# Kernel tuning notes

Hardware: AMD Instinct MI355X
Metric: run time of the kernel (lower is better)

Reference implementation:

```python
import jax, jax.numpy as jnp
import numpy as np

B, S, H = 2, 2048, 2048
NH = 16
HD = H // NH  # 128


def setup_inputs() -> dict:
    key = jax.random.key(0)
    ks = jax.random.split(key, 6)
    sc = 0.02
    return {
        "x": jax.random.normal(ks[0], (B, S, H), dtype=jnp.float32),
        "attention_mask": jnp.zeros((B, S), dtype=jnp.float32),
        "Wq": jax.random.normal(ks[1], (H, H), dtype=jnp.float32) * sc,
        "bq": jnp.zeros((H,), dtype=jnp.float32),
        "Wk": jax.random.normal(ks[2], (H, H), dtype=jnp.float32) * sc,
        "bk": jnp.zeros((H,), dtype=jnp.float32),
        "Wv": jax.random.normal(ks[3], (H, H), dtype=jnp.float32) * sc,
        "bv": jnp.zeros((H,), dtype=jnp.float32),
        "Wo": jax.random.normal(ks[4], (H, H), dtype=jnp.float32) * sc,
        "bo": jnp.zeros((H,), dtype=jnp.float32),
    }


def reference(x, attention_mask, Wq, bq, Wk, bk, Wv, bv, Wo, bo):
    b, s, h = x.shape
    q = (x @ Wq + bq).reshape(b, s, NH, HD)
    k = (x @ Wk + bk).reshape(b, s, NH, HD)
    v = (x @ Wv + bv).reshape(b, s, NH, HD)
    scale = 1.0 / jnp.sqrt(jnp.asarray(HD, dtype=x.dtype))
    scores = jnp.einsum('bqhd,bkhd->bhqk', q, k) * scale
    scores = scores + attention_mask[:, None, None, :]
    weights = jax.nn.softmax(scores, axis=-1)
    attn = jnp.einsum('bhqk,bkhd->bqhd', weights, v).reshape(b, s, h)
    return attn @ Wo + bo
```

## Files before the change

kernel.cpp:

```cpp
#include <hip/hip_runtime.h>
#include <hip/hip_bf16.h>
#include <stdint.h>

#define BB   2
#define SS   2048
#define HHH  2048
#define NHH  16
#define HDD  128
#define MTOT 4096

typedef __bf16 bf16x8 __attribute__((ext_vector_type(8)));
typedef float  f32x4  __attribute__((ext_vector_type(4)));
typedef float  f32x16 __attribute__((ext_vector_type(16)));

#define MFMA16(a, b, c) __builtin_amdgcn_mfma_f32_16x16x32_bf16((a), (b), (c), 0, 0, 0)
#define MFMA32(a, b, c) __builtin_amdgcn_mfma_f32_32x32x16_bf16((a), (b), (c), 0, 0, 0)

__device__ __forceinline__ unsigned short f2bf(float f) {
    union { float f; unsigned u; } v; v.f = f;
    unsigned r = v.u + 0x7FFFu + ((v.u >> 16) & 1u);
    return (unsigned short)(r >> 16);
}

__device__ __forceinline__ unsigned packbf(float a, float b) {
    union { __bf16 h[2]; unsigned u; } p;
    p.h[0] = (__bf16)a; p.h[1] = (__bf16)b;
    return p.u;
}

__device__ __forceinline__ void pswap(unsigned &a, unsigned &b) {
    asm("v_permlane32_swap_b32 %0, %1" : "+v"(a), "+v"(b));
}

__device__ __forceinline__ float2 xswap(float x) {
    unsigned a = __builtin_bit_cast(unsigned, x);
    unsigned b;
    asm("v_mov_b32 %0, %1" : "=v"(b) : "v"(a));
    asm("v_permlane32_swap_b32 %0, %1" : "+v"(a), "+v"(b));
    return make_float2(__builtin_bit_cast(float, a), __builtin_bit_cast(float, b));
}

__device__ __forceinline__ void gload16(const void* src, void* lds) {
    __builtin_amdgcn_global_load_lds(
        (__attribute__((address_space(1))) void*)src,
        (__attribute__((address_space(3))) void*)lds,
        16, 0, 0);
}

__global__ void cast_f32_bf16(const float* __restrict__ in,
                              unsigned short* __restrict__ out, int n) {
    int i = (blockIdx.x * blockDim.x + threadIdx.x) * 4;
    int stride = gridDim.x * blockDim.x * 4;
    for (; i < n; i += stride) {
        float4 v = *(const float4*)(in + i);
        ushort4 o;
        o.x = f2bf(v.x); o.y = f2bf(v.y); o.z = f2bf(v.z); o.w = f2bf(v.w);
        *(ushort4*)(out + i) = o;
    }
}

__global__ void scale_mask(const float* __restrict__ in, float* __restrict__ out) {
    int i = blockIdx.x * 256 + threadIdx.x;
    out[i] = in[i] * 1.4426950408889634f;
}

__global__ void transpose_cast4(const float* __restrict__ W0, const float* __restrict__ W1,
                                const float* __restrict__ W2, const float* __restrict__ W3,
                                unsigned short* __restrict__ out) {
    const float* in = blockIdx.z == 0 ? W0 : blockIdx.z == 1 ? W1 : blockIdx.z == 2 ? W2 : W3;
    unsigned short* o = out + (size_t)blockIdx.z * ((size_t)HHH * HHH);
    __shared__ float tile[32][33];
    int c0 = blockIdx.x * 32, r0 = blockIdx.y * 32;
    int tx = threadIdx.x, ty = threadIdx.y;
    #pragma unroll
    for (int i = 0; i < 32; i += 8)
        tile[ty + i][tx] = in[(size_t)(r0 + ty + i) * HHH + c0 + tx];
    __syncthreads();
    #pragma unroll
    for (int i = 0; i < 32; i += 8)
        o[(size_t)(c0 + ty + i) * HHH + r0 + tx] = f2bf(tile[tx][ty + i]);
}

template<int MODE>
__global__ __launch_bounds__(512, 2) void gemm8_bf16(
    const unsigned short* __restrict__ A,
    const unsigned short* __restrict__ Bt,
    const float* __restrict__ bias,
    void* __restrict__ Cout,
    int M, int N, int K)
{
    __shared__ __align__(16) unsigned char sm[147456];
    const int tid = threadIdx.x;
    const int wv = tid >> 6, ln = tid & 63;
    const int g = ln >> 4, r = ln & 15;
    const int wr = wv >> 2, wc = wv & 3;

    const int bid = blockIdx.x;
    const int lb = (bid & 7) * 32 + (bid >> 3);
    const int m0 = (lb & 31) * 128;
    const int n0 = (lb >> 5) * 256;

    unsigned srcA[2]; int ldsA[2];
    #pragma unroll
    for (int j = 0; j < 2; ++j) {
        int o = j * 8192 + tid * 16;
        int row = o >> 7;
        int lg = ((o >> 4) & 7) ^ (row & 7);
        srcA[j] = (unsigned)(m0 + row) * K + lg * 8;
        ldsA[j] = o;
    }
    unsigned srcB[4]; int ldsB[4];
    #pragma unroll
    for (int j = 0; j < 4; ++j) {
        int o = j * 8192 + tid * 16;
        int row = o >> 7;
        int lg = ((o >> 4) & 7) ^ (row & 7);
        srcB[j] = (unsigned)(n0 + row) * K + lg * 8;
        ldsB[j] = 16384 + o;
    }

    f32x4 acc[4][4];
    #pragma unroll
    for (int i = 0; i < 4; ++i)
        #pragma unroll
        for (int j = 0; j < 4; ++j)
            acc[i][j] = (f32x4){0.f, 0.f, 0.f, 0.f};

    const int NT = K >> 6;

    {
        unsigned char* b0 = sm;
        unsigned char* b1 = sm + 49152;
        #pragma unroll
        for (int j = 0; j < 2; ++j) gload16(A + srcA[j], b0 + ldsA[j]);
        #pragma unroll
        for (int j = 0; j < 4; ++j) gload16(Bt + srcB[j], b0 + ldsB[j]);
        #pragma unroll
        for (int j = 0; j < 2; ++j) gload16(A + srcA[j] + 64, b1 + ldsA[j]);
        #pragma unroll
        for (int j = 0; j < 4; ++j) gload16(Bt + srcB[j] + 64, b1 + ldsB[j]);
    }
    asm volatile("s_waitcnt vmcnt(6)" ::: "memory");
    __builtin_amdgcn_s_barrier();

    int csel = 0;
    int psel = 2;
    for (int t = 0; t < NT; ++t) {
        const unsigned char* Ab = sm + csel * 49152;
        const unsigned char* Bb = Ab + 16384;
        unsigned char* Pb = sm + psel * 49152;
        const bool pre = (t + 2 < NT);
        const int ko = (t + 2) * 64;

        bf16x8 af[2][2], bf[2][2];
        #define LDA(mi, ks) (*(const bf16x8*)(Ab + (wr * 64 + (mi) * 16 + r) * 128 + \
                             ((((ks) << 2) + g) ^ ((wr * 64 + (mi) * 16 + r) & 7)) * 16))
        #define LDB(ni, ks) (*(const bf16x8*)(Bb + (wc * 64 + (ni) * 16 + r) * 128 + \
                             ((((ks) << 2) + g) ^ ((wc * 64 + (ni) * 16 + r) & 7)) * 16))

        af[0][0] = LDA(0, 0); af[0][1] = LDA(0, 1);
        af[1][0] = LDA(1, 0); af[1][1] = LDA(1, 1);
        bf[0][0] = LDB(0, 0); bf[0][1] = LDB(0, 1);
        bf[1][0] = LDB(1, 0); bf[1][1] = LDB(1, 1);
        if (pre) { gload16(Bt + srcB[0] + ko, Pb + ldsB[0]);
                   gload16(Bt + srcB[1] + ko, Pb + ldsB[1]); }
        __builtin_amdgcn_s_barrier();
        asm volatile("s_waitcnt lgkmcnt(0)" ::: "memory");
        __builtin_amdgcn_s_setprio(1);
        #pragma unroll
        for (int mi = 0; mi < 2; ++mi)
            #pragma unroll
            for (int ni = 0; ni < 2; ++ni)
                #pragma unroll
                for (int ks = 0; ks < 2; ++ks)
                    acc[mi][ni] = MFMA16(af[mi][ks], bf[ni][ks], acc[mi][ni]);
        __builtin_amdgcn_s_setprio(0);
        __builtin_amdgcn_s_barrier();

        bf[0][0] = LDB(2, 0); bf[0][1] = LDB(2, 1);
        bf[1][0] = LDB(3, 0); bf[1][1] = LDB(3, 1);
        if (pre) { gload16(Bt + srcB[2] + ko, Pb + ldsB[2]);
                   gload16(Bt + srcB[3] + ko, Pb + ldsB[3]); }
        __builtin_amdgcn_s_barrier();
        asm volatile("s_waitcnt lgkmcnt(0)" ::: "memory");
        __builtin_amdgcn_s_setprio(1);
        #pragma unroll
        for (int mi = 0; mi < 2; ++mi)
            #pragma unroll
            for (int ni = 0; ni < 2; ++ni)
                #pragma unroll
                for (int ks = 0; ks < 2; ++ks)
                    acc[mi][ni + 2] = MFMA16(af[mi][ks], bf[ni][ks], acc[mi][ni + 2]);
        __builtin_amdgcn_s_setprio(0);
        __builtin_amdgcn_s_barrier();

        af[0][0] = LDA(2, 0); af[0][1] = LDA(2, 1);
        af[1][0] = LDA(3, 0); af[1][1] = LDA(3, 1);
        if (pre) { gload16(A + srcA[0] + ko, Pb + ldsA[0]);
                   gload16(A + srcA[1] + ko, Pb + ldsA[1]); }
        __builtin_amdgcn_s_barrier();
        asm volatile("s_waitcnt lgkmcnt(0)" ::: "memory");
        __builtin_amdgcn_s_setprio(1);
        #pragma unroll
        for (int mi = 0; mi < 2; ++mi)
            #pragma unroll
            for (int ni = 0; ni < 2; ++ni)
                #pragma unroll
                for (int ks = 0; ks < 2; ++ks)
                    acc[mi + 2][ni + 2] = MFMA16(af[mi][ks], bf[ni][ks], acc[mi + 2][ni + 2]);
        __builtin_amdgcn_s_setprio(0);
        __builtin_amdgcn_s_barrier();

        bf[0][0] = LDB(0, 0); bf[0][1] = LDB(0, 1);
        bf[1][0] = LDB(1, 0); bf[1][1] = LDB(1, 1);
        __builtin_amdgcn_s_barrier();
        asm volatile("s_waitcnt lgkmcnt(0)" ::: "memory");
        __builtin_amdgcn_s_setprio(1);
        #pragma unroll
        for (int mi = 0; mi < 2; ++mi)
            #pragma unroll
            for (int ni = 0; ni < 2; ++ni)
                #pragma unroll
                for (int ks = 0; ks < 2; ++ks)
                    acc[mi + 2][ni] = MFMA16(af[mi][ks], bf[ni][ks], acc[mi + 2][ni]);
        __builtin_amdgcn_s_setprio(0);
        __builtin_amdgcn_s_barrier();

        if (pre) asm volatile("s_waitcnt vmcnt(6)" ::: "memory");
        else     asm volatile("s_waitcnt vmcnt(0)" ::: "memory");
        __builtin_amdgcn_s_barrier();

        csel = (csel == 2) ? 0 : csel + 1;
        psel = (psel == 2) ? 0 : psel + 1;
        #undef LDA
        #undef LDB
    }

    #pragma unroll
    for (int mt = 0; mt < 4; ++mt) {
        #pragma unroll
        for (int nt = 0; nt < 4; ++nt) {
            int col = n0 + wc * 64 + nt * 16 + r;
            float bvv = bias[col];
            f32x4 a = acc[mt][nt];
            int mrow = m0 + wr * 64 + mt * 16 + g * 4;
            if (MODE == 0) {
                #pragma unroll
                for (int q = 0; q < 4; ++q)
                    ((unsigned short*)Cout)[(size_t)(mrow + q) * N + col] = f2bf(a[q] + bvv);
            } else if (MODE == 2) {
                #pragma unroll
                for (int q = 0; q < 4; ++q)
                    ((float*)Cout)[(size_t)(mrow + q) * N + col] = a[q] + bvv;
            } else {
                int b = mrow >> 11, s0x = mrow & 2047;
                ushort4 o;
                o.x = f2bf(a[0] + bvv); o.y = f2bf(a[1] + bvv);
                o.z = f2bf(a[2] + bvv); o.w = f2bf(a[3] + bvv);
                *(ushort4*)((unsigned short*)Cout + ((size_t)(b * 2048 + col)) * 2048 + s0x) = o;
            }
        }
    }
}

__global__ __launch_bounds__(256, 2) void attn_fwd(
    const unsigned short* __restrict__ Q,
    const unsigned short* __restrict__ K,
    const unsigned short* __restrict__ V,
    const float* __restrict__ maskl2,
    unsigned short* __restrict__ O)
{
    __shared__ __align__(16) unsigned char sm[49152];
    const int tid = threadIdx.x, wv = tid >> 6, ln = tid & 63;
    const int hi = ln >> 5, qr = ln & 31;

    const int bid = blockIdx.x;
    const int lb = (bid & 7) * 64 + (bid >> 3);
    const int qb = lb & 15;
    const int bh = lb >> 4;
    const int h = bh & 15, b = bh >> 4;

    const size_t rowQ0 = (size_t)(b * 2048 + qb * 128 + wv * 32);
    const float SCL2 = 0.08838834764831845f * 1.4426950408889634f;

    unsigned srcK[2], srcV[2];
    int ldsK[2], ldsV[2];
    #pragma unroll
    for (int i = 0; i < 2; ++i) {
        int ch = wv * 2 + i;
        int o = ch * 1024 + ln * 16;
        { int row = o >> 8; int gl = ((o >> 4) & 15) ^ (row & 7);
          srcK[i] = (unsigned)((b * 2048 + row) * 2048 + h * 128 + gl * 8);
          ldsK[i] = o; }
        { int d = o >> 6; int gl = ((o >> 4) & 3) ^ ((d >> 1) & 3);
          srcV[i] = (unsigned)((b * 2048 + h * 128 + d) * 2048 + gl * 8);
          ldsV[i] = 8192 + o; }
    }

    #define STAGE(t, base) { \
        _Pragma("unroll") \
        for (int i = 0; i < 2; ++i) { \
            gload16(K + srcK[i] + (unsigned)(t) * (32u * 2048u), sm + (base) + ldsK[i]); \
            gload16(V + srcV[i] + (unsigned)(t) * 32u, sm + (base) + ldsV[i]); \
        } }

    STAGE(0, 0); STAGE(1, 16384); STAGE(2, 32768);

    bf16x8 qf[8];
    #pragma unroll
    for (int ks = 0; ks < 8; ++ks)
        qf[ks] = *(const bf16x8*)(Q + (rowQ0 + qr) * 2048 + h * 128 + ks * 16 + hi * 8);

    f32x16 acc[4];
    #pragma unroll
    for (int i = 0; i < 4; ++i)
        #pragma unroll
        for (int j = 0; j < 16; ++j)
            acc[i][j] = 0.f;
    float mr = -3.0e38f, lr = 0.f;

    const float* mb = maskl2 + b * 2048;

    asm volatile("s_waitcnt vmcnt(8)" ::: "memory");
    __builtin_amdgcn_s_barrier();

    int bufo = 0;
    for (int t = 0; t < 64; ++t) {
        const unsigned char* Kt = sm + bufo;
        const unsigned char* Vt = Kt + 8192;

        f32x4 mk[4];
        #pragma unroll
        for (int rg = 0; rg < 4; ++rg)
            mk[rg] = *(const f32x4*)(mb + t * 32 + rg * 8 + hi * 4);

        f32x16 sf;
        #pragma unroll
        for (int j = 0; j < 16; ++j) sf[j] = 0.f;
        __builtin_amdgcn_s_setprio(1);
        #pragma unroll
        for (int ks = 0; ks < 8; ++ks) {
            int s0 = (2 * ks + hi) ^ (qr & 7);
            bf16x8 kf = *(const bf16x8*)(Kt + qr * 256 + s0 * 16);
            sf = MFMA32(kf, qf[ks], sf);
        }
        __builtin_amdgcn_s_setprio(0);

        float sv[16];
        #pragma unroll
        for (int reg = 0; reg < 16; ++reg)
            sv[reg] = sf[reg] * SCL2 + mk[reg >> 2][reg & 3];

        float mx[8];
        #pragma unroll
        for (int j = 0; j < 8; ++j)
            mx[j] = fmaxf(sv[2 * j], sv[2 * j + 1]);
        float m01 = fmaxf(fmaxf(fmaxf(mx[0], mx[1]), fmaxf(mx[2], mx[3])),
                          fmaxf(fmaxf(mx[4], mx[5]), fmaxf(mx[6], mx[7])));
        float2 mp = xswap(m01);
        float mt = fmaxf(mp.x, mp.y);

        float alpha = 1.f;
        int allskip = __all(mt <= mr + 8.f);
        if (!allskip) {
            float nm = fmaxf(mr, mt);
            alpha = __builtin_amdgcn_exp2f(mr - nm);
            mr = nm;
            #pragma unroll
            for (int dblk = 0; dblk < 4; ++dblk)
                #pragma unroll
                for (int reg = 0; reg < 16; ++reg)
                    acc[dblk][reg] *= alpha;
        }

        float s0 = 0.f, s1 = 0.f, s2 = 0.f, s3 = 0.f;
        #pragma unroll
        for (int reg = 0; reg < 16; reg += 4) {
            float p0 = __builtin_amdgcn_exp2f(sv[reg + 0] - mr);
            float p1 = __builtin_amdgcn_exp2f(sv[reg + 1] - mr);
            float p2 = __builtin_amdgcn_exp2f(sv[reg + 2] - mr);
            float p3 = __builtin_amdgcn_exp2f(sv[reg + 3] - mr);
            sv[reg + 0] = p0; sv[reg + 1] = p1;
            sv[reg + 2] = p2; sv[reg + 3] = p3;
            s0 += p0; s1 += p1; s2 += p2; s3 += p3;
        }
        float rsl = (s0 + s1) + (s2 + s3);
        float2 rp = xswap(rsl);
        float rs = rp.x + rp.y;
        lr = lr * alpha + rs;

        bf16x8 pfr[2];
        #pragma unroll
        for (int kb16 = 0; kb16 < 2; ++kb16) {
            unsigned W00 = packbf(sv[(2*kb16+0)*4 + 0], sv[(2*kb16+0)*4 + 1]);
            unsigned W01 = packbf(sv[(2*kb16+0)*4 + 2], sv[(2*kb16+0)*4 + 3]);
            unsigned W10 = packbf(sv[(2*kb16+1)*4 + 0], sv[(2*kb16+1)*4 + 1]);
            unsigned W11 = packbf(sv[(2*kb16+1)*4 + 2], sv[(2*kb16+1)*4 + 3]);
            pswap(W00, W10);
            pswap(W01, W11);
            union { unsigned w[4]; bf16x8 v; } u;
            u.w[0] = W00; u.w[1] = W01; u.w[2] = W10; u.w[3] = W11;
            pfr[kb16] = u.v;
        }

        __builtin_amdgcn_s_setprio(1);
        #pragma unroll
        for (int dblk = 0; dblk < 4; ++dblk) {
            int d = dblk * 32 + qr;
            f32x16 a = acc[dblk];
            #pragma unroll
            for (int kb16 = 0; kb16 < 2; ++kb16) {
                int s = (2 * kb16 + hi) ^ ((d >> 1) & 3);
                bf16x8 vf = *(const bf16x8*)(Vt + d * 64 + s * 16);
                a = MFMA32(vf, pfr[kb16], a);
            }
            acc[dblk] = a;
        }
        __builtin_amdgcn_s_setprio(0);

        asm volatile("s_waitcnt vmcnt(4)" ::: "memory");
        __builtin_amdgcn_s_barrier();

        if (t + 3 < 64) STAGE(t + 3, bufo);
        bufo = (bufo == 32768) ? 0 : bufo + 16384;
    }

    float linv = 1.f / lr;
    unsigned short* orow = O + (rowQ0 + qr) * 2048 + h * 128;
    #pragma unroll
    for (int dblk = 0; dblk < 4; ++dblk)
        #pragma unroll
        for (int rg = 0; rg < 4; ++rg) {
            float v0 = acc[dblk][rg * 4 + 0] * linv;
            float v1 = acc[dblk][rg * 4 + 1] * linv;
            float v2 = acc[dblk][rg * 4 + 2] * linv;
            float v3 = acc[dblk][rg * 4 + 3] * linv;
            uint2 o;
            o.x = packbf(v0, v1);
            o.y = packbf(v2, v3);
            *(uint2*)(orow + dblk * 32 + rg * 8 + hi * 4) = o;
        }
    #undef STAGE
}

extern "C" void kernel_launch(void* const* d_in, const int* in_sizes, int n_in,
                              void* d_out, int out_size, void* d_ws, size_t ws_size,
                              hipStream_t stream)
{
    (void)in_sizes; (void)n_in; (void)out_size; (void)ws_size;
    const float* x    = (const float*)d_in[0];
    const float* mask = (const float*)d_in[1];
    const float* Wq   = (const float*)d_in[2];
    const float* bq   = (const float*)d_in[3];
    const float* Wk   = (const float*)d_in[4];
    const float* bk   = (const float*)d_in[5];
    const float* Wv   = (const float*)d_in[6];
    const float* bv   = (const float*)d_in[7];
    const float* Wo   = (const float*)d_in[8];
    const float* bo   = (const float*)d_in[9];
    float* out = (float*)d_out;

    char* ws = (char*)d_ws;
    unsigned short* xb  = (unsigned short*)(ws);
    unsigned short* Wqt = (unsigned short*)(ws + (16u << 20));
    unsigned short* Wkt = (unsigned short*)(ws + (24u << 20));
    unsigned short* Wvt = (unsigned short*)(ws + (32u << 20));
    unsigned short* Wot = (unsigned short*)(ws + (40u << 20));
    unsigned short* Qb  = (unsigned short*)(ws + (48u << 20));
    unsigned short* Kb  = (unsigned short*)(ws + (64u << 20));
    unsigned short* Vtb = (unsigned short*)(ws + (80u << 20));
    unsigned short* Ab  = (unsigned short*)(ws + (16u << 20));
    float*          mkl = (float*)(ws + (32u << 20));

    cast_f32_bf16<<<2048, 256, 0, stream>>>(x, xb, MTOT * HHH);
    transpose_cast4<<<dim3(64, 64, 4), dim3(32, 8), 0, stream>>>(Wq, Wk, Wv, Wo, Wqt);

    gemm8_bf16<0><<<256, 512, 0, stream>>>(xb, Wqt, bq, Qb,  MTOT, HHH, HHH);
    gemm8_bf16<0><<<256, 512, 0, stream>>>(xb, Wkt, bk, Kb,  MTOT, HHH, HHH);
    gemm8_bf16<1><<<256, 512, 0, stream>>>(xb, Wvt, bv, Vtb, MTOT, HHH, HHH);

    scale_mask<<<(BB * SS) / 256, 256, 0, stream>>>(mask, mkl);
    attn_fwd<<<512, 256, 0, stream>>>(Qb, Kb, Vtb, mkl, Ab);

    gemm8_bf16<2><<<256, 512, 0, stream>>>(Ab, Wot, bo, out, MTOT, HHH, HHH);
}
```

Baseline: 291.6 us.

## Merge GEMM MFMA phases, stage attention mask in LDS, split QK accumulators

The GEMM main loop goes from four barrier-separated MFMA phases to two. All four B fragments are loaded up front and the global prefetches are redistributed, which cuts barrier count but raises register pressure. In the attention kernel, the per-batch mask row is copied into shared memory once, so each tile no longer reads it from global memory. The QK^T MFMA chain is split into two independent accumulators to shorten the dependency chain, at the cost of extra registers and a final add. Shared memory for attention grows, which may affect occupancy.

```diff
diff --git a/kernel.cpp b/kernel.cpp
--- a/kernel.cpp
+++ b/kernel.cpp
@@ -152,7 +152,7 @@
         const bool pre = (t + 2 < NT);
         const int ko = (t + 2) * 64;
 
-        bf16x8 af[2][2], bf[2][2];
+        bf16x8 af[2][2], bfr[4][2];
         #define LDA(mi, ks) (*(const bf16x8*)(Ab + (wr * 64 + (mi) * 16 + r) * 128 + \
                              ((((ks) << 2) + g) ^ ((wr * 64 + (mi) * 16 + r) & 7)) * 16))
         #define LDB(ni, ks) (*(const bf16x8*)(Bb + (wc * 64 + (ni) * 16 + r) * 128 + \
@@ -160,43 +160,31 @@
 
         af[0][0] = LDA(0, 0); af[0][1] = LDA(0, 1);
         af[1][0] = LDA(1, 0); af[1][1] = LDA(1, 1);
-        bf[0][0] = LDB(0, 0); bf[0][1] = LDB(0, 1);
-        bf[1][0] = LDB(1, 0); bf[1][1] = LDB(1, 1);
+        #pragma unroll
+        for (int ni = 0; ni < 4; ++ni) {
+            bfr[ni][0] = LDB(ni, 0);
+            bfr[ni][1] = LDB(ni, 1);
+        }
         if (pre) { gload16(Bt + srcB[0] + ko, Pb + ldsB[0]);
-                   gload16(Bt + srcB[1] + ko, Pb + ldsB[1]); }
+                   gload16(Bt + srcB[1] + ko, Pb + ldsB[1]);
+                   gload16(Bt + srcB[2] + ko, Pb + ldsB[2]); }
         __builtin_amdgcn_s_barrier();
         asm volatile("s_waitcnt lgkmcnt(0)" ::: "memory");
         __builtin_amdgcn_s_setprio(1);
         #pragma unroll
         for (int mi = 0; mi < 2; ++mi)
             #pragma unroll
-            for (int ni = 0; ni < 2; ++ni)
+            for (int ni = 0; ni < 4; ++ni)
                 #pragma unroll
                 for (int ks = 0; ks < 2; ++ks)
-                    acc[mi][ni] = MFMA16(af[mi][ks], bf[ni][ks], acc[mi][ni]);
+                    acc[mi][ni] = MFMA16(af[mi][ks], bfr[ni][ks], acc[mi][ni]);
         __builtin_amdgcn_s_setprio(0);
         __builtin_amdgcn_s_barrier();
 
-        bf[0][0] = LDB(2, 0); bf[0][1] = LDB(2, 1);
-        bf[1][0] = LDB(3, 0); bf[1][1] = LDB(3, 1);
-        if (pre) { gload16(Bt + srcB[2] + ko, Pb + ldsB[2]);
-                   gload16(Bt + srcB[3] + ko, Pb + ldsB[3]); }
-        __builtin_amdgcn_s_barrier();
-        asm volatile("s_waitcnt lgkmcnt(0)" ::: "memory");
-        __builtin_amdgcn_s_setprio(1);
-        #pragma unroll
-        for (int mi = 0; mi < 2; ++mi)
-            #pragma unroll
-            for (int ni = 0; ni < 2; ++ni)
-                #pragma unroll
-                for (int ks = 0; ks < 2; ++ks)
-                    acc[mi][ni + 2] = MFMA16(af[mi][ks], bf[ni][ks], acc[mi][ni + 2]);
-        __builtin_amdgcn_s_setprio(0);
-        __builtin_amdgcn_s_barrier();
-
         af[0][0] = LDA(2, 0); af[0][1] = LDA(2, 1);
         af[1][0] = LDA(3, 0); af[1][1] = LDA(3, 1);
-        if (pre) { gload16(A + srcA[0] + ko, Pb + ldsA[0]);
+        if (pre) { gload16(Bt + srcB[3] + ko, Pb + ldsB[3]);
+                   gload16(A + srcA[0] + ko, Pb + ldsA[0]);
                    gload16(A + srcA[1] + ko, Pb + ldsA[1]); }
         __builtin_amdgcn_s_barrier();
         asm volatile("s_waitcnt lgkmcnt(0)" ::: "memory");
@@ -204,27 +192,11 @@
         #pragma unroll
         for (int mi = 0; mi < 2; ++mi)
             #pragma unroll
-            for (int ni = 0; ni < 2; ++ni)
+            for (int ni = 0; ni < 4; ++ni)
                 #pragma unroll
                 for (int ks = 0; ks < 2; ++ks)
-                    acc[mi + 2][ni + 2] = MFMA16(af[mi][ks], bf[ni][ks], acc[mi + 2][ni + 2]);
+                    acc[mi + 2][ni] = MFMA16(af[mi][ks], bfr[ni][ks], acc[mi + 2][ni]);
         __builtin_amdgcn_s_setprio(0);
-        __builtin_amdgcn_s_barrier();
-
-        bf[0][0] = LDB(0, 0); bf[0][1] = LDB(0, 1);
-        bf[1][0] = LDB(1, 0); bf[1][1] = LDB(1, 1);
-        __builtin_amdgcn_s_barrier();
-        asm volatile("s_waitcnt lgkmcnt(0)" ::: "memory");
-        __builtin_amdgcn_s_setprio(1);
-        #pragma unroll
-        for (int mi = 0; mi < 2; ++mi)
-            #pragma unroll
-            for (int ni = 0; ni < 2; ++ni)
-                #pragma unroll
-                for (int ks = 0; ks < 2; ++ks)
-                    acc[mi + 2][ni] = MFMA16(af[mi][ks], bf[ni][ks], acc[mi + 2][ni]);
-        __builtin_amdgcn_s_setprio(0);
-        __builtin_amdgcn_s_barrier();
 
         if (pre) asm volatile("s_waitcnt vmcnt(6)" ::: "memory");
         else     asm volatile("s_waitcnt vmcnt(0)" ::: "memory");
@@ -270,7 +242,7 @@
     const float* __restrict__ maskl2,
     unsigned short* __restrict__ O)
 {
-    __shared__ __align__(16) unsigned char sm[49152];
+    __shared__ __align__(16) unsigned char sm[57344];
     const int tid = threadIdx.x, wv = tid >> 6, ln = tid & 63;
     const int hi = ln >> 5, qr = ln & 31;
 
@@ -304,6 +276,10 @@
             gload16(V + srcV[i] + (unsigned)(t) * 32u, sm + (base) + ldsV[i]); \
         } }
 
+    #pragma unroll
+    for (int i = 0; i < 2; ++i)
+        gload16(maskl2 + b * 2048 + wv * 512 + i * 256 + ln * 4,
+                sm + 49152 + wv * 2048 + i * 1024);
     STAGE(0, 0); STAGE(1, 16384); STAGE(2, 32768);
 
     bf16x8 qf[8];
@@ -319,7 +295,7 @@
             acc[i][j] = 0.f;
     float mr = -3.0e38f, lr = 0.f;
 
-    const float* mb = maskl2 + b * 2048;
+    const float* ml = (const float*)(sm + 49152);
 
     asm volatile("s_waitcnt vmcnt(8)" ::: "memory");
     __builtin_amdgcn_s_barrier();
@@ -332,24 +308,30 @@
         f32x4 mk[4];
         #pragma unroll
         for (int rg = 0; rg < 4; ++rg)
-            mk[rg] = *(const f32x4*)(mb + t * 32 + rg * 8 + hi * 4);
-
-        f32x16 sf;
-        #pragma unroll
-        for (int j = 0; j < 16; ++j) sf[j] = 0.f;
+            mk[rg] = *(const f32x4*)(ml + t * 32 + rg * 8 + hi * 4);
+
+        f32x16 sfA, sfB;
+        #pragma unroll
+        for (int j = 0; j < 16; ++j) { sfA[j] = 0.f; sfB[j] = 0.f; }
         __builtin_amdgcn_s_setprio(1);
         #pragma unroll
-        for (int ks = 0; ks < 8; ++ks) {
+        for (int ks = 0; ks < 4; ++ks) {
             int s0 = (2 * ks + hi) ^ (qr & 7);
             bf16x8 kf = *(const bf16x8*)(Kt + qr * 256 + s0 * 16);
-            sf = MFMA32(kf, qf[ks], sf);
+            sfA = MFMA32(kf, qf[ks], sfA);
+        }
+        #pragma unroll
+        for (int ks = 4; ks < 8; ++ks) {
+            int s0 = (2 * ks + hi) ^ (qr & 7);
+            bf16x8 kf = *(const bf16x8*)(Kt + qr * 256 + s0 * 16);
+            sfB = MFMA32(kf, qf[ks], sfB);
         }
         __builtin_amdgcn_s_setprio(0);
 
         float sv[16];
         #pragma unroll
         for (int reg = 0; reg < 16; ++reg)
-            sv[reg] = sf[reg] * SCL2 + mk[reg >> 2][reg & 3];
+            sv[reg] = (sfA[reg] + sfB[reg]) * SCL2 + mk[reg >> 2][reg & 3];
 
         float mx[8];
         #pragma unroll
```

After: 279.6 us. 4.1% less time.
